# Kernel tuning notes

Hardware: AMD Instinct MI355X
Metric: run time of the kernel (lower is better)

The kernel has to match this reference:

```python
import jax, jax.numpy as jnp
import numpy as np

N = 131072
CODE_DIM = 64
HIDDEN = 128
DT_MAX = 0.125
N_STEPS = 8  # = ceil(max|t1-t2| / DT_MAX); extra steps are exact no-ops since dt=0 for finished rows


def setup_inputs() -> dict:
    key = jax.random.key(0)
    ks = jax.random.split(key, 8)
    deform_code = jax.random.normal(ks[0], (N, CODE_DIM), dtype=jnp.float32)
    pos_init = jax.random.normal(ks[1], (N, 3), dtype=jnp.float32)
    t1 = jax.random.uniform(ks[2], (N, 1), dtype=jnp.float32)
    t2 = jnp.zeros((N, 1), dtype=jnp.float32)
    # vel_net MLP params: concat(code, xyzt)[68] -> 128 -> 128 -> 3, tanh activations
    s1 = 1.0 / np.sqrt(CODE_DIM + 4)
    s2 = 1.0 / np.sqrt(HIDDEN)
    W1 = jax.random.normal(ks[3], (CODE_DIM + 4, HIDDEN), dtype=jnp.float32) * s1
    b1 = jnp.zeros((HIDDEN,), dtype=jnp.float32)
    W2 = jax.random.normal(ks[4], (HIDDEN, HIDDEN), dtype=jnp.float32) * s2
    b2 = jnp.zeros((HIDDEN,), dtype=jnp.float32)
    W3 = jax.random.normal(ks[5], (HIDDEN, 3), dtype=jnp.float32) * s2
    b3 = jnp.zeros((3,), dtype=jnp.float32)
    return {"deform_code": deform_code, "pos_init": pos_init, "t1": t1, "t2": t2,
            "W1": W1, "b1": b1, "W2": W2, "b2": b2, "W3": W3, "b3": b3}


def reference(deform_code, pos_init, t1, t2, W1, b1, W2, b2, W3, b3):
    def get_vel(code, xyzt):  # works for single sample or batch
        x = jnp.concatenate([code, xyzt], axis=-1)
        h = jnp.tanh(x @ W1 + b1)
        h = jnp.tanh(h @ W2 + b2)
        return h @ W3 + b3

    def u_func(code, xyzt):  # per-sample, for jacobian wrt xyzt (argnums=1)
        u = get_vel(code, xyzt)
        return u, u

    jac_fn = jax.vmap(jax.jacrev(u_func, argnums=1, has_aux=True))  # [N,3,4] jac, [N,3] vel

    n = pos_init.shape[0]
    deform0 = jnp.broadcast_to(jnp.eye(3, dtype=pos_init.dtype), (n, 3, 3))

    def step(state, _):
        xyz, t_curr, offset, deform = state
        # dt == 0 exactly for finished rows -> all updates below are no-ops (matches masked in-place updates)
        dt = jnp.sign(offset) * jnp.minimum(jnp.abs(offset), DT_MAX)  # [N,1]
        v0 = get_vel(deform_code, jnp.concatenate([xyz, t_curr], axis=-1))
        p_mid = xyz - 0.5 * dt * v0
        t_mid = t_curr - 0.5 * dt
        jac_v, velocity = jac_fn(deform_code, jnp.concatenate([p_mid, t_mid], axis=-1))
        drotdt = jnp.einsum('noi,nij->noj', jac_v[:, :3, :3], deform)
        deform = deform - dt[..., None] * drotdt
        xyz = xyz - dt * velocity
        return (xyz, t_curr - dt, offset - dt, deform), None

    state0 = (pos_init, t1, t1 - t2, deform0)
    (xyz, _, _, deform), _ = jax.lax.scan(step, state0, None, length=N_STEPS)
    return xyz, deform
```

## Files before the change

### kernel.cpp

```cpp
#include <hip/hip_runtime.h>
#include <hip/hip_bf16.h>

#define H 128
#define NSTEPS 8
#define DT_MAXF 0.125f
#define WAVES 4
#define PPW 16
#define PPB (WAVES*PPW)
#define WPACK_U4 4992

typedef __attribute__((ext_vector_type(8))) short short8;
typedef __attribute__((ext_vector_type(4))) float floatx4;
typedef __attribute__((ext_vector_type(2))) float f32x2;

__device__ __forceinline__ f32x2 sp2(float v) { return (f32x2){v, v}; }
__device__ __forceinline__ f32x2 fma2(f32x2 a, f32x2 b, f32x2 c) {
    return __builtin_elementwise_fma(a, b, c);
}
__device__ __forceinline__ f32x2 tanh2(f32x2 x) {
    f32x2 y = x * 2.8853900817779268f;
    f32x2 e; e[0] = __builtin_amdgcn_exp2f(y[0]); e[1] = __builtin_amdgcn_exp2f(y[1]);
    f32x2 ep = e + 1.0f;
    float rt = __builtin_amdgcn_rcpf(ep[0] * ep[1]);
    f32x2 eps = __builtin_shufflevector(ep, ep, 1, 0);
    f32x2 r = eps * sp2(rt);
    return fma2(sp2(-2.0f), r, sp2(1.0f));
}
__device__ __forceinline__ unsigned f2bf(float x) {
    unsigned u = __float_as_uint(x);
    return (u + 0x7FFFu + ((u >> 16) & 1u)) >> 16;
}
__device__ __forceinline__ unsigned pk2(float a, float b) {
    union { __hip_bfloat162 h; unsigned u; } U;
    U.h = __float22bfloat162_rn(make_float2(a, b));
    return U.u;
}
__device__ __forceinline__ unsigned pkv(f32x2 v) { return pk2(v[0], v[1]); }
__device__ __forceinline__ short8 mk8(unsigned a, unsigned b, unsigned c, unsigned d) {
    union { unsigned u[4]; short8 s; } U;
    U.u[0] = a; U.u[1] = b; U.u[2] = c; U.u[3] = d; return U.s;
}
__device__ __forceinline__ short8 xyzt_frag(float x, float y, float z, float t, int q) {
    unsigned hx = f2bf(x), hy = f2bf(y), hz = f2bf(z), ht = f2bf(t);
    float lx = x - __uint_as_float(hx << 16);
    float ly = y - __uint_as_float(hy << 16);
    float lz = z - __uint_as_float(hz << 16);
    float lt = t - __uint_as_float(ht << 16);
    unsigned w0 = hx | (hy << 16), w1 = hz | (ht << 16);
    unsigned w2 = pk2(lx, ly),     w3 = pk2(lz, lt);
    union { unsigned u[4]; short8 s; } F;
    F.u[0] = (q < 2)  ? w0 : 0u;
    F.u[1] = (q < 2)  ? w1 : 0u;
    F.u[2] = (q == 0) ? w2 : 0u;
    F.u[3] = (q == 0) ? w3 : 0u;
    return F.s;
}

__device__ __forceinline__ int step_bucket(float t1v, float t2v) {
    float off = fabsf(t1v - t2v);
    int b = (int)ceilf(off * 8.0f);
    return min(max(b, 0), 8);
}
__global__ void prep_hist(const float* __restrict__ t1g, const float* __restrict__ t2g,
                          unsigned* cnt, int N) {
    __shared__ unsigned h[9];
    if (threadIdx.x < 9) h[threadIdx.x] = 0u;
    __syncthreads();
    int i = blockIdx.x * 256 + threadIdx.x;
    if (i < N) atomicAdd(&h[step_bucket(t1g[i], t2g[i])], 1u);
    __syncthreads();
    if (threadIdx.x < 9 && h[threadIdx.x]) atomicAdd(&cnt[threadIdx.x], h[threadIdx.x]);
}
__global__ void prep_prefix(unsigned* cnt) {
    if (threadIdx.x == 0) {
        unsigned run = 0;
        for (int b = 8; b >= 0; --b) { unsigned c = cnt[b]; cnt[9 + b] = run; run += c; }
    }
}
__global__ void prep_scatter(const float* __restrict__ t1g, const float* __restrict__ t2g,
                             unsigned* cnt, int* __restrict__ perm, int N) {
    __shared__ unsigned h[9];
    __shared__ unsigned base[9];
    if (threadIdx.x < 9) h[threadIdx.x] = 0u;
    __syncthreads();
    int i = blockIdx.x * 256 + threadIdx.x;
    int b = 0; unsigned r = 0;
    if (i < N) {
        b = step_bucket(t1g[i], t2g[i]);
        r = atomicAdd(&h[b], 1u);
    }
    __syncthreads();
    if (threadIdx.x < 9 && h[threadIdx.x])
        base[threadIdx.x] = atomicAdd(&cnt[9 + threadIdx.x], h[threadIdx.x]);
    __syncthreads();
    if (i < N) perm[base[b] + r] = i;
}

__global__ void prep_pack(const float* __restrict__ W1, const float* __restrict__ W2,
                          const float* __restrict__ W3, const float* __restrict__ b2,
                          uint4* __restrict__ wp) {
    const int gid = blockIdx.x * 256 + threadIdx.x;
    const int stride = gridDim.x * 256;
    for (int e = gid; e < 1024; e += stride) {
        int t = e >> 7, rem = e & 127;
        int c = rem >> 6, l = rem & 63;
        int qq = l >> 4, mm = l & 15;
        int u = t*16 + mm;
        int g0 = c*32 + qq*4, g1 = g0 + 16;
        unsigned hh[8]; float lo[8];
        #pragma unroll
        for (int j = 0; j < 4; ++j) {
            float w0 = W1[(g0+j)*H + u];
            float w1 = W1[(g1+j)*H + u];
            hh[j]   = f2bf(w0); lo[j]   = w0 - __uint_as_float(hh[j]   << 16);
            hh[4+j] = f2bf(w1); lo[4+j] = w1 - __uint_as_float(hh[4+j] << 16);
        }
        wp[((t*2+c)*2+0)*64 + l] = make_uint4(hh[0]|(hh[1]<<16), hh[2]|(hh[3]<<16),
                                              hh[4]|(hh[5]<<16), hh[6]|(hh[7]<<16));
        wp[((t*2+c)*2+1)*64 + l] = make_uint4(pk2(lo[0],lo[1]), pk2(lo[2],lo[3]),
                                              pk2(lo[4],lo[5]), pk2(lo[6],lo[7]));
    }
    for (int ch = gid; ch < 2048; ch += stride) {
        int ln = ch & 63, ts = ch >> 6;
        int s = ts & 3, t = ts >> 2;
        int qq = ln >> 4, n = t*16 + (ln & 15);
        int u0 = s*32 + qq*4, u1 = u0 + 16;
        unsigned w0 = f2bf(W2[(u0+0)*H+n]) | (f2bf(W2[(u0+1)*H+n]) << 16);
        unsigned w1 = f2bf(W2[(u0+2)*H+n]) | (f2bf(W2[(u0+3)*H+n]) << 16);
        unsigned w2 = f2bf(W2[(u1+0)*H+n]) | (f2bf(W2[(u1+1)*H+n]) << 16);
        unsigned w3v = f2bf(W2[(u1+2)*H+n]) | (f2bf(W2[(u1+3)*H+n]) << 16);
        wp[2048 + ch] = make_uint4(w0, w1, w2, w3v);
    }
    for (int e = gid; e < 512; e += stride) {
        int t = e >> 6, l = e & 63;
        int u = t*16 + (l & 15), qq = l >> 4;
        unsigned hb[4], lb[4];
        #pragma unroll
        for (int c = 0; c < 4; ++c) {
            float wv = W1[(64 + c)*H + u];
            unsigned hh = f2bf(wv);
            float wl = wv - __uint_as_float(hh << 16);
            hb[c] = hh; lb[c] = f2bf(wl);
        }
        unsigned hi01 = hb[0] | (hb[1] << 16), hi23 = hb[2] | (hb[3] << 16);
        unsigned lo01 = lb[0] | (lb[1] << 16), lo23 = lb[2] | (lb[3] << 16);
        uint4 o;
        if (qq == 0)      o = make_uint4(hi01, hi23, hi01, hi23);
        else if (qq == 1) o = make_uint4(lo01, lo23, 0u, 0u);
        else              o = make_uint4(0u, 0u, 0u, 0u);
        wp[4096 + e] = o;
    }
    for (int e = gid; e < 256; e += stride) {
        int s = e >> 6, l = e & 63;
        int a = l & 15, qq = l >> 4;
        uint4 o = make_uint4(0u, 0u, 0u, 0u);
        if (a < 3) {
            int u0 = s*32 + qq*4, u1 = u0 + 16;
            o.x = f2bf(W3[(u0+0)*3+a]) | (f2bf(W3[(u0+1)*3+a]) << 16);
            o.y = f2bf(W3[(u0+2)*3+a]) | (f2bf(W3[(u0+3)*3+a]) << 16);
            o.z = f2bf(W3[(u1+0)*3+a]) | (f2bf(W3[(u1+1)*3+a]) << 16);
            o.w = f2bf(W3[(u1+2)*3+a]) | (f2bf(W3[(u1+3)*3+a]) << 16);
        }
        wp[4608 + e] = o;
    }
    for (int i = gid; i < 128; i += stride) {
        int sec = i >> 5, k = i & 31;
        float4 v = (sec < 3) ? ((const float4*)(W1 + (size_t)(64+sec)*H))[k]
                             : ((const float4*)b2)[k];
        wp[4864 + i] = *(const uint4*)&v;
    }
}

__global__ __launch_bounds__(256, 2)
void velwarp(const float* __restrict__ code, const float* __restrict__ pos,
             const float* __restrict__ t1g, const float* __restrict__ t2g,
             const float* __restrict__ W1, const float* __restrict__ b1,
             const float* __restrict__ W2, const float* __restrict__ b2,
             const float* __restrict__ W3, const float* __restrict__ b3,
             float* __restrict__ out, const int* __restrict__ perm,
             const uint4* __restrict__ wpack, int N)
{
    __shared__ __align__(16) uint4 WbufU[2048];
    __shared__ __align__(16) uint4 W1AU[8*64];
    __shared__ __align__(16) uint4 W3AU[4*64];
    __shared__ __align__(16) floatx4 WdX4[32];
    __shared__ __align__(16) floatx4 WdY4[32];
    __shared__ __align__(16) floatx4 WdZ4[32];
    __shared__ __align__(16) floatx4 b2C4[32];

    const int tid = threadIdx.x;
    const int L   = tid & 63;
    const int m   = L & 15;
    const int q   = L >> 4;
    const int pb  = blockIdx.x * PPB + (tid >> 6) * PPW;
    const int p   = perm ? perm[pb + m] : (pb + m);

    if (wpack) {
        #pragma unroll 4
        for (int i = tid; i < 2048; i += 256) WbufU[i] = wpack[i];
        #pragma unroll 2
        for (int i = tid; i < 512; i += 256) W1AU[i] = wpack[4096 + i];
        W3AU[tid < 256 ? tid : 0] = wpack[4608 + (tid < 256 ? tid : 0)];
        if (tid < 128) {
            int sec = tid >> 5, k = tid & 31;
            uint4 v = wpack[4864 + tid];
            floatx4 f = *(const floatx4*)&v;
            if (sec == 0)      WdX4[k] = f;
            else if (sec == 1) WdY4[k] = f;
            else if (sec == 2) WdZ4[k] = f;
            else               b2C4[k] = f;
        }
    } else {
        for (int e = tid; e < 1024; e += 256) {
            int t = e >> 7, rem = e & 127;
            int c = rem >> 6, l = rem & 63;
            int qq = l >> 4, mm = l & 15;
            int u = t*16 + mm;
            int g0 = c*32 + qq*4, g1 = g0 + 16;
            unsigned hh[8]; float lo[8];
            #pragma unroll
            for (int j = 0; j < 4; ++j) {
                float w0 = W1[(g0+j)*H + u];
                float w1 = W1[(g1+j)*H + u];
                hh[j]   = f2bf(w0); lo[j]   = w0 - __uint_as_float(hh[j]   << 16);
                hh[4+j] = f2bf(w1); lo[4+j] = w1 - __uint_as_float(hh[4+j] << 16);
            }
            WbufU[((t*2+c)*2+0)*64 + l] = make_uint4(hh[0]|(hh[1]<<16), hh[2]|(hh[3]<<16),
                                                     hh[4]|(hh[5]<<16), hh[6]|(hh[7]<<16));
            WbufU[((t*2+c)*2+1)*64 + l] = make_uint4(pk2(lo[0],lo[1]), pk2(lo[2],lo[3]),
                                                     pk2(lo[4],lo[5]), pk2(lo[6],lo[7]));
        }
        for (int e = tid; e < 512; e += 256) {
            int t = e >> 6, l = e & 63;
            int u = t*16 + (l & 15), qq = l >> 4;
            unsigned hb[4], lb[4];
            #pragma unroll
            for (int c = 0; c < 4; ++c) {
                float wv = W1[(64 + c)*H + u];
                unsigned hh = f2bf(wv);
                float wl = wv - __uint_as_float(hh << 16);
                hb[c] = hh; lb[c] = f2bf(wl);
            }
            unsigned hi01 = hb[0] | (hb[1] << 16), hi23 = hb[2] | (hb[3] << 16);
            unsigned lo01 = lb[0] | (lb[1] << 16), lo23 = lb[2] | (lb[3] << 16);
            uint4 o;
            if (qq == 0)      o = make_uint4(hi01, hi23, hi01, hi23);
            else if (qq == 1) o = make_uint4(lo01, lo23, 0u, 0u);
            else              o = make_uint4(0u, 0u, 0u, 0u);
            W1AU[e] = o;
        }
        for (int e = tid; e < 256; e += 256) {
            int s = e >> 6, l = e & 63;
            int a = l & 15, qq = l >> 4;
            uint4 o = make_uint4(0u, 0u, 0u, 0u);
            if (a < 3) {
                int u0 = s*32 + qq*4, u1 = u0 + 16;
                o.x = f2bf(W3[(u0+0)*3+a]) | (f2bf(W3[(u0+1)*3+a]) << 16);
                o.y = f2bf(W3[(u0+2)*3+a]) | (f2bf(W3[(u0+3)*3+a]) << 16);
                o.z = f2bf(W3[(u1+0)*3+a]) | (f2bf(W3[(u1+1)*3+a]) << 16);
                o.w = f2bf(W3[(u1+2)*3+a]) | (f2bf(W3[(u1+3)*3+a]) << 16);
            }
            W3AU[e] = o;
        }
        if (tid < 32) {
            WdX4[tid] = ((const floatx4*)(W1 + (size_t)64*H))[tid];
            WdY4[tid] = ((const floatx4*)(W1 + (size_t)65*H))[tid];
            WdZ4[tid] = ((const floatx4*)(W1 + (size_t)66*H))[tid];
            b2C4[tid] = ((const floatx4*)b2)[tid];
        }
    }
    __syncthreads();

    floatx4 base1C[8];
    {
        const float4* crow4 = (const float4*)(code + (size_t)p * 64);
        short8 Bh[2], Bl[2];
        #pragma unroll
        for (int c = 0; c < 2; ++c) {
            float4 a = crow4[c*8 + q];
            float4 b = crow4[c*8 + 4 + q];
            unsigned h0 = f2bf(a.x), h1 = f2bf(a.y), h2 = f2bf(a.z), h3 = f2bf(a.w);
            unsigned g0 = f2bf(b.x), g1 = f2bf(b.y), g2 = f2bf(b.z), g3 = f2bf(b.w);
            float l0 = a.x - __uint_as_float(h0<<16), l1 = a.y - __uint_as_float(h1<<16);
            float l2 = a.z - __uint_as_float(h2<<16), l3 = a.w - __uint_as_float(h3<<16);
            float m0 = b.x - __uint_as_float(g0<<16), m1 = b.y - __uint_as_float(g1<<16);
            float m2 = b.z - __uint_as_float(g2<<16), m3 = b.w - __uint_as_float(g3<<16);
            Bh[c] = mk8(h0|(h1<<16), h2|(h3<<16), g0|(g1<<16), g2|(g3<<16));
            Bl[c] = mk8(pk2(l0,l1), pk2(l2,l3), pk2(m0,m1), pk2(m2,m3));
        }
        const short8* Wb = (const short8*)WbufU;
        #pragma unroll
        for (int t = 0; t < 8; ++t) {
            floatx4 z = *(const floatx4*)&b1[t*16 + q*4];
            short8 Wh0 = Wb[((t*2+0)*2+0)*64 + L];
            short8 Wh1 = Wb[((t*2+1)*2+0)*64 + L];
            short8 Wl0 = Wb[((t*2+0)*2+1)*64 + L];
            short8 Wl1 = Wb[((t*2+1)*2+1)*64 + L];
            z = __builtin_amdgcn_mfma_f32_16x16x32_bf16(Wh0, Bh[0], z, 0, 0, 0);
            z = __builtin_amdgcn_mfma_f32_16x16x32_bf16(Wh1, Bh[1], z, 0, 0, 0);
            z = __builtin_amdgcn_mfma_f32_16x16x32_bf16(Wh0, Bl[0], z, 0, 0, 0);
            z = __builtin_amdgcn_mfma_f32_16x16x32_bf16(Wh1, Bl[1], z, 0, 0, 0);
            z = __builtin_amdgcn_mfma_f32_16x16x32_bf16(Wl0, Bh[0], z, 0, 0, 0);
            z = __builtin_amdgcn_mfma_f32_16x16x32_bf16(Wl1, Bh[1], z, 0, 0, 0);
            base1C[t] = z;
        }
    }
    __syncthreads();

    if (wpack) {
        #pragma unroll 4
        for (int i = tid; i < 2048; i += 256) WbufU[i] = wpack[2048 + i];
    } else {
        for (int ch = tid; ch < 2048; ch += 256) {
            int ln = ch & 63, ts = ch >> 6;
            int s = ts & 3, t = ts >> 2;
            int qq = ln >> 4, n = t*16 + (ln & 15);
            int u0 = s*32 + qq*4, u1 = u0 + 16;
            unsigned w0 = f2bf(W2[(u0+0)*H+n]) | (f2bf(W2[(u0+1)*H+n]) << 16);
            unsigned w1 = f2bf(W2[(u0+2)*H+n]) | (f2bf(W2[(u0+3)*H+n]) << 16);
            unsigned w2 = f2bf(W2[(u1+0)*H+n]) | (f2bf(W2[(u1+1)*H+n]) << 16);
            unsigned w3v = f2bf(W2[(u1+2)*H+n]) | (f2bf(W2[(u1+3)*H+n]) << 16);
            WbufU[ch] = make_uint4(w0, w1, w2, w3v);
        }
    }

    float px_ = pos[p*3+0], py_ = pos[p*3+1], pz_ = pos[p*3+2];
    float tc_ = t1g[p];
    float off_ = tc_ - t2g[p];
    f32x2 Dp[3]; float Ds[3];
    Dp[0] = (f32x2){1.f, 0.f}; Ds[0] = 0.f;
    Dp[1] = (f32x2){0.f, 1.f}; Ds[1] = 0.f;
    Dp[2] = (f32x2){0.f, 0.f}; Ds[2] = 1.f;
    const float b30 = b3[0], b31 = b3[1], b32 = b3[2];
    __syncthreads();

    const short8* Bf   = (const short8*)WbufU;
    const short8* W1Af = (const short8*)W1AU;
    const short8* W3Af = (const short8*)W3AU;
    const floatx4 Z4 = {0.f, 0.f, 0.f, 0.f};

    for (int step = 0; step < NSTEPS; ++step) {
        if (!__any(off_ != 0.0f)) break;

        float vAx, vAy, vAz;
        {
            short8 xf = xyzt_frag(px_, py_, pz_, tc_, q);
            floatx4 z[8];
            #pragma unroll
            for (int t = 0; t < 8; ++t)
                z[t] = __builtin_amdgcn_mfma_f32_16x16x32_bf16(W1Af[t*64 + L], xf, base1C[t], 0, 0, 0);
            short8 fh[4];
            #pragma unroll
            for (int s = 0; s < 4; ++s) {
                f32x2 a0 = tanh2(z[2*s].xy),   a1 = tanh2(z[2*s].zw);
                f32x2 c0 = tanh2(z[2*s+1].xy), c1 = tanh2(z[2*s+1].zw);
                fh[s] = mk8(pkv(a0), pkv(a1), pkv(c0), pkv(c1));
            }
            __builtin_amdgcn_sched_barrier(0);
            floatx4 vacc = Z4;
            #pragma unroll
            for (int qi = 0; qi < 4; ++qi) {
                const int T0 = 2*qi, T1 = 2*qi + 1;
                floatx4 acc0 = __builtin_amdgcn_mfma_f32_16x16x32_bf16(
                    Bf[(T0*4 + 0)*64 + L], fh[0], b2C4[T0*4 + q], 0, 0, 0);
                floatx4 acc1 = __builtin_amdgcn_mfma_f32_16x16x32_bf16(
                    Bf[(T1*4 + 0)*64 + L], fh[0], b2C4[T1*4 + q], 0, 0, 0);
                #pragma unroll
                for (int s = 1; s < 4; ++s) {
                    acc0 = __builtin_amdgcn_mfma_f32_16x16x32_bf16(Bf[(T0*4 + s)*64 + L], fh[s], acc0, 0, 0, 0);
                    acc1 = __builtin_amdgcn_mfma_f32_16x16x32_bf16(Bf[(T1*4 + s)*64 + L], fh[s], acc1, 0, 0, 0);
                }
                f32x2 e00 = tanh2(acc0.xy), e01 = tanh2(acc0.zw);
                f32x2 e10 = tanh2(acc1.xy), e11 = tanh2(acc1.zw);
                short8 ef = mk8(pkv(e00), pkv(e01), pkv(e10), pkv(e11));
                vacc = __builtin_amdgcn_mfma_f32_16x16x32_bf16(W3Af[qi*64 + L], ef, vacc, 0, 0, 0);
                __builtin_amdgcn_sched_barrier(0);
            }
            vAx = __shfl(vacc[0], m, 64);
            vAy = __shfl(vacc[1], m, 64);
            vAz = __shfl(vacc[2], m, 64);
        }

        float dt_ = copysignf(fminf(fabsf(off_), DT_MAXF), off_);
        float hd = 0.5f * dt_;
        float mx = px_ - hd*(vAx + b30);
        float my = py_ - hd*(vAy + b31);
        float mz = pz_ - hd*(vAz + b32);
        float tm = tc_ - hd;

        float vx, vy, vz;
        floatx4 V = Z4, J0 = Z4, J1 = Z4, J2 = Z4;
        {
            short8 xf = xyzt_frag(mx, my, mz, tm, q);
            floatx4 z[8];
            #pragma unroll
            for (int t = 0; t < 8; ++t)
                z[t] = __builtin_amdgcn_mfma_f32_16x16x32_bf16(W1Af[t*64 + L], xf, base1C[t], 0, 0, 0);
            short8 fh[4], fd0[4], fd1[4], fd2[4];
            #pragma unroll
            for (int s = 0; s < 4; ++s) {
                unsigned uh[4], u0[4], u1[4], u2[4];
                #pragma unroll
                for (int hf = 0; hf < 2; ++hf) {
                    int t = 2*s + hf;
                    f32x2 h0 = tanh2(z[t].xy), h1 = tanh2(z[t].zw);
                    f32x2 s0 = fma2(-h0, h0, sp2(1.0f));
                    f32x2 s1 = fma2(-h1, h1, sp2(1.0f));
                    floatx4 wx = WdX4[t*4 + q], wy = WdY4[t*4 + q], wz = WdZ4[t*4 + q];
                    uh[2*hf+0] = pkv(h0);         uh[2*hf+1] = pkv(h1);
                    u0[2*hf+0] = pkv(s0 * wx.xy); u0[2*hf+1] = pkv(s1 * wx.zw);
                    u1[2*hf+0] = pkv(s0 * wy.xy); u1[2*hf+1] = pkv(s1 * wy.zw);
                    u2[2*hf+0] = pkv(s0 * wz.xy); u2[2*hf+1] = pkv(s1 * wz.zw);
                }
                fh[s]  = mk8(uh[0], uh[1], uh[2], uh[3]);
                fd0[s] = mk8(u0[0], u0[1], u0[2], u0[3]);
                fd1[s] = mk8(u1[0], u1[1], u1[2], u1[3]);
                fd2[s] = mk8(u2[0], u2[1], u2[2], u2[3]);
            }
            __builtin_amdgcn_sched_barrier(0);
            #pragma unroll
            for (int qi = 0; qi < 4; ++qi) {
                const int T0 = 2*qi, T1 = 2*qi + 1;
                floatx4 aH0, aH1, aD00, aD01, aD10, aD11, aD20, aD21;
                {
                    short8 A0 = Bf[(T0*4 + 0)*64 + L];
                    short8 A1 = Bf[(T1*4 + 0)*64 + L];
                    aH0  = __builtin_amdgcn_mfma_f32_16x16x32_bf16(A0, fh[0],  b2C4[T0*4 + q], 0, 0, 0);
                    aH1  = __builtin_amdgcn_mfma_f32_16x16x32_bf16(A1, fh[0],  b2C4[T1*4 + q], 0, 0, 0);
                    aD00 = __builtin_amdgcn_mfma_f32_16x16x32_bf16(A0, fd0[0], Z4, 0, 0, 0);
                    aD01 = __builtin_amdgcn_mfma_f32_16x16x32_bf16(A1, fd0[0], Z4, 0, 0, 0);
                    aD10 = __builtin_amdgcn_mfma_f32_16x16x32_bf16(A0, fd1[0], Z4, 0, 0, 0);
                    aD11 = __builtin_amdgcn_mfma_f32_16x16x32_bf16(A1, fd1[0], Z4, 0, 0, 0);
                    aD20 = __builtin_amdgcn_mfma_f32_16x16x32_bf16(A0, fd2[0], Z4, 0, 0, 0);
                    aD21 = __builtin_amdgcn_mfma_f32_16x16x32_bf16(A1, fd2[0], Z4, 0, 0, 0);
                }
                #pragma unroll
                for (int s = 1; s < 4; ++s) {
                    short8 A0 = Bf[(T0*4 + s)*64 + L];
                    short8 A1 = Bf[(T1*4 + s)*64 + L];
                    aH0  = __builtin_amdgcn_mfma_f32_16x16x32_bf16(A0, fh[s],  aH0,  0, 0, 0);
                    aH1  = __builtin_amdgcn_mfma_f32_16x16x32_bf16(A1, fh[s],  aH1,  0, 0, 0);
                    aD00 = __builtin_amdgcn_mfma_f32_16x16x32_bf16(A0, fd0[s], aD00, 0, 0, 0);
                    aD01 = __builtin_amdgcn_mfma_f32_16x16x32_bf16(A1, fd0[s], aD01, 0, 0, 0);
                    aD10 = __builtin_amdgcn_mfma_f32_16x16x32_bf16(A0, fd1[s], aD10, 0, 0, 0);
                    aD11 = __builtin_amdgcn_mfma_f32_16x16x32_bf16(A1, fd1[s], aD11, 0, 0, 0);
                    aD20 = __builtin_amdgcn_mfma_f32_16x16x32_bf16(A0, fd2[s], aD20, 0, 0, 0);
                    aD21 = __builtin_amdgcn_mfma_f32_16x16x32_bf16(A1, fd2[s], aD21, 0, 0, 0);
                }
                f32x2 h0 = tanh2(aH0.xy), h1 = tanh2(aH0.zw);
                f32x2 h2v = tanh2(aH1.xy), h3 = tanh2(aH1.zw);
                f32x2 s0 = fma2(-h0, h0, sp2(1.0f));
                f32x2 s1 = fma2(-h1, h1, sp2(1.0f));
                f32x2 s2v = fma2(-h2v, h2v, sp2(1.0f));
                f32x2 s3 = fma2(-h3, h3, sp2(1.0f));
                short8 eh = mk8(pkv(h0), pkv(h1), pkv(h2v), pkv(h3));
                short8 e0 = mk8(pkv(s0*aD00.xy), pkv(s1*aD00.zw), pkv(s2v*aD01.xy), pkv(s3*aD01.zw));
                short8 e1 = mk8(pkv(s0*aD10.xy), pkv(s1*aD10.zw), pkv(s2v*aD11.xy), pkv(s3*aD11.zw));
                short8 e2 = mk8(pkv(s0*aD20.xy), pkv(s1*aD20.zw), pkv(s2v*aD21.xy), pkv(s3*aD21.zw));
                const short8 WA = W3Af[qi*64 + L];
                V  = __builtin_amdgcn_mfma_f32_16x16x32_bf16(WA, eh, V,  0, 0, 0);
                J0 = __builtin_amdgcn_mfma_f32_16x16x32_bf16(WA, e0, J0, 0, 0, 0);
                J1 = __builtin_amdgcn_mfma_f32_16x16x32_bf16(WA, e1, J1, 0, 0, 0);
                J2 = __builtin_amdgcn_mfma_f32_16x16x32_bf16(WA, e2, J2, 0, 0, 0);
                __builtin_amdgcn_sched_barrier(0);
            }
            vx = __shfl(V[0], m, 64) + b30;
            vy = __shfl(V[1], m, 64) + b31;
            vz = __shfl(V[2], m, 64) + b32;
        }

        {
            f32x2 ndp[3]; float nds[3];
            #pragma unroll
            for (int o = 0; o < 3; ++o) {
                f32x2 tp = J0[o] * Dp[0];
                tp = fma2(sp2(J1[o]), Dp[1], tp);
                tp = fma2(sp2(J2[o]), Dp[2], tp);
                ndp[o] = fma2(sp2(-dt_), tp, Dp[o]);
                float ts = J0[o]*Ds[0];
                ts = fmaf(J1[o], Ds[1], ts);
                ts = fmaf(J2[o], Ds[2], ts);
                nds[o] = fmaf(-dt_, ts, Ds[o]);
            }
            #pragma unroll
            for (int o = 0; o < 3; ++o) { Dp[o] = ndp[o]; Ds[o] = nds[o]; }
        }
        px_ = fmaf(-dt_, vx, px_);
        py_ = fmaf(-dt_, vy, py_);
        pz_ = fmaf(-dt_, vz, pz_);
        tc_  -= dt_;
        off_ -= dt_;
    }

    if (q == 0) {
        out[p*3+0] = px_; out[p*3+1] = py_; out[p*3+2] = pz_;
        float* o9 = out + (size_t)N*3 + (size_t)p*9;
        #pragma unroll
        for (int o = 0; o < 3; ++o) {
            o9[o*3+0] = Dp[o][0];
            o9[o*3+1] = Dp[o][1];
            o9[o*3+2] = Ds[o];
        }
    }
}

extern "C" void kernel_launch(void* const* d_in, const int* in_sizes, int n_in,
                              void* d_out, int out_size, void* d_ws, size_t ws_size,
                              hipStream_t stream) {
    const float* code = (const float*)d_in[0];
    const float* pos  = (const float*)d_in[1];
    const float* t1   = (const float*)d_in[2];
    const float* t2   = (const float*)d_in[3];
    const float* W1   = (const float*)d_in[4];
    const float* b1   = (const float*)d_in[5];
    const float* W2   = (const float*)d_in[6];
    const float* b2   = (const float*)d_in[7];
    const float* W3   = (const float*)d_in[8];
    const float* b3   = (const float*)d_in[9];
    float* out = (float*)d_out;
    const int N = in_sizes[1] / 3;
    const int blocks = N / PPB;
    const int pblocks = (N + 255) / 256;

    const size_t need_perm = 128 + (size_t)N * sizeof(int);
    const size_t need_full = 128 + (size_t)WPACK_U4 * 16 + (size_t)N * sizeof(int);
    int* perm = nullptr;
    uint4* wpack = nullptr;
    if (d_ws && ws_size >= need_full) {
        unsigned* cnt = (unsigned*)d_ws;
        wpack = (uint4*)((char*)d_ws + 128);
        perm  = (int*)((char*)d_ws + 128 + (size_t)WPACK_U4 * 16);
        hipMemsetAsync(d_ws, 0, 128, stream);
        prep_pack<<<20, 256, 0, stream>>>(W1, W2, W3, b2, wpack);
        prep_hist<<<pblocks, 256, 0, stream>>>(t1, t2, cnt, N);
        prep_prefix<<<1, 64, 0, stream>>>(cnt);
        prep_scatter<<<pblocks, 256, 0, stream>>>(t1, t2, cnt, perm, N);
    } else if (d_ws && ws_size >= need_perm) {
        unsigned* cnt = (unsigned*)d_ws;
        perm = (int*)((char*)d_ws + 128);
        hipMemsetAsync(d_ws, 0, 128, stream);
        prep_hist<<<pblocks, 256, 0, stream>>>(t1, t2, cnt, N);
        prep_prefix<<<1, 64, 0, stream>>>(cnt);
        prep_scatter<<<pblocks, 256, 0, stream>>>(t1, t2, cnt, perm, N);
    }
    velwarp<<<blocks, 256, 0, stream>>>(code, pos, t1, t2, W1, b1, W2, b2, W3, b3,
                                        out, perm, wpack, N);
}
```

Baseline: 272.8 us.

## Fuse prep kernels into two launches and compute layer-1 base from global weights

Replaces the memset plus four prep launches (pack, hist, prefix, scatter) with two kernels. The first kernel computes per-block bucket histograms and does the weight packing in extra blocks. The second kernel has each block rebuild its own exclusive prefix from all block counts, so no global atomics or separate prefix kernel are needed. In the main kernel, the layer-1 code projection now reads packed W1 straight from global memory, which lets W2 be loaded into shared memory once with fewer barriers. The trade-offs are a redundant per-block prefix scan over 512 blocks and uncached global reads of W1 fragments.

```diff
diff --git a/kernel.cpp b/kernel.cpp
--- a/kernel.cpp
+++ b/kernel.cpp
@@ -8,6 +8,8 @@
 #define PPW 16
 #define PPB (WAVES*PPW)
 #define WPACK_U4 4992
+#define HBLK 512
+#define PACKB 20
 
 typedef __attribute__((ext_vector_type(8))) short short8;
 typedef __attribute__((ext_vector_type(4))) float floatx4;
@@ -61,46 +63,11 @@
     int b = (int)ceilf(off * 8.0f);
     return min(max(b, 0), 8);
 }
-__global__ void prep_hist(const float* __restrict__ t1g, const float* __restrict__ t2g,
-                          unsigned* cnt, int N) {
-    __shared__ unsigned h[9];
-    if (threadIdx.x < 9) h[threadIdx.x] = 0u;
-    __syncthreads();
-    int i = blockIdx.x * 256 + threadIdx.x;
-    if (i < N) atomicAdd(&h[step_bucket(t1g[i], t2g[i])], 1u);
-    __syncthreads();
-    if (threadIdx.x < 9 && h[threadIdx.x]) atomicAdd(&cnt[threadIdx.x], h[threadIdx.x]);
-}
-__global__ void prep_prefix(unsigned* cnt) {
-    if (threadIdx.x == 0) {
-        unsigned run = 0;
-        for (int b = 8; b >= 0; --b) { unsigned c = cnt[b]; cnt[9 + b] = run; run += c; }
-    }
-}
-__global__ void prep_scatter(const float* __restrict__ t1g, const float* __restrict__ t2g,
-                             unsigned* cnt, int* __restrict__ perm, int N) {
-    __shared__ unsigned h[9];
-    __shared__ unsigned base[9];
-    if (threadIdx.x < 9) h[threadIdx.x] = 0u;
-    __syncthreads();
-    int i = blockIdx.x * 256 + threadIdx.x;
-    int b = 0; unsigned r = 0;
-    if (i < N) {
-        b = step_bucket(t1g[i], t2g[i]);
-        r = atomicAdd(&h[b], 1u);
-    }
-    __syncthreads();
-    if (threadIdx.x < 9 && h[threadIdx.x])
-        base[threadIdx.x] = atomicAdd(&cnt[9 + threadIdx.x], h[threadIdx.x]);
-    __syncthreads();
-    if (i < N) perm[base[b] + r] = i;
-}
-
-__global__ void prep_pack(const float* __restrict__ W1, const float* __restrict__ W2,
+
+__device__ void pack_body(int gid, int stride,
+                          const float* __restrict__ W1, const float* __restrict__ W2,
                           const float* __restrict__ W3, const float* __restrict__ b2,
                           uint4* __restrict__ wp) {
-    const int gid = blockIdx.x * 256 + threadIdx.x;
-    const int stride = gridDim.x * 256;
     for (int e = gid; e < 1024; e += stride) {
         int t = e >> 7, rem = e & 127;
         int c = rem >> 6, l = rem & 63;
@@ -169,6 +136,91 @@
                              : ((const float4*)b2)[k];
         wp[4864 + i] = *(const uint4*)&v;
     }
+}
+
+__global__ void prep_hist2(const float* __restrict__ t1g, const float* __restrict__ t2g,
+                           unsigned* __restrict__ cnt2, int N, int pblocks,
+                           const float* __restrict__ W1, const float* __restrict__ W2,
+                           const float* __restrict__ W3, const float* __restrict__ b2,
+                           uint4* __restrict__ wp) {
+    if ((int)blockIdx.x >= pblocks) {
+        pack_body((blockIdx.x - pblocks)*256 + threadIdx.x, PACKB*256, W1, W2, W3, b2, wp);
+        return;
+    }
+    __shared__ unsigned h[9];
+    if (threadIdx.x < 9) h[threadIdx.x] = 0u;
+    __syncthreads();
+    int i = blockIdx.x * 256 + threadIdx.x;
+    if (i < N) atomicAdd(&h[step_bucket(t1g[i], t2g[i])], 1u);
+    __syncthreads();
+    if (threadIdx.x < 9) cnt2[blockIdx.x*9 + threadIdx.x] = h[threadIdx.x];
+}
+__global__ void prep_scatter2(const float* __restrict__ t1g, const float* __restrict__ t2g,
+                              const unsigned* __restrict__ cnt2, int* __restrict__ perm,
+                              int N, int pblocks) {
+    __shared__ unsigned cs[HBLK*9];
+    __shared__ unsigned T9[9], O9[9], base9[9], alloc9[9];
+    const int b = blockIdx.x, tid = threadIdx.x;
+    for (int i = tid; i < pblocks*9; i += 256) cs[i] = cnt2[i];
+    if (tid < 9) alloc9[tid] = 0u;
+    __syncthreads();
+    if (tid < 9) {
+        unsigned O = 0, T = 0;
+        for (int i = 0; i < pblocks; ++i) {
+            unsigned c = cs[i*9 + tid];
+            if (i < b) O += c;
+            T += c;
+        }
+        T9[tid] = T; O9[tid] = O;
+    }
+    __syncthreads();
+    if (tid < 9) {
+        unsigned G = 0;
+        for (int k = 8; k > tid; --k) G += T9[k];
+        base9[tid] = G + O9[tid];
+    }
+    __syncthreads();
+    int i = b*256 + tid;
+    if (i < N) {
+        int k = step_bucket(t1g[i], t2g[i]);
+        unsigned r = atomicAdd(&alloc9[k], 1u);
+        perm[base9[k] + r] = i;
+    }
+}
+
+__global__ void prep_hist(const float* __restrict__ t1g, const float* __restrict__ t2g,
+                          unsigned* cnt, int N) {
+    __shared__ unsigned h[9];
+    if (threadIdx.x < 9) h[threadIdx.x] = 0u;
+    __syncthreads();
+    int i = blockIdx.x * 256 + threadIdx.x;
+    if (i < N) atomicAdd(&h[step_bucket(t1g[i], t2g[i])], 1u);
+    __syncthreads();
+    if (threadIdx.x < 9 && h[threadIdx.x]) atomicAdd(&cnt[threadIdx.x], h[threadIdx.x]);
+}
+__global__ void prep_prefix(unsigned* cnt) {
+    if (threadIdx.x == 0) {
+        unsigned run = 0;
+        for (int b = 8; b >= 0; --b) { unsigned c = cnt[b]; cnt[9 + b] = run; run += c; }
+    }
+}
+__global__ void prep_scatter(const float* __restrict__ t1g, const float* __restrict__ t2g,
+                             unsigned* cnt, int* __restrict__ perm, int N) {
+    __shared__ unsigned h[9];
+    __shared__ unsigned base[9];
+    if (threadIdx.x < 9) h[threadIdx.x] = 0u;
+    __syncthreads();
+    int i = blockIdx.x * 256 + threadIdx.x;
+    int b = 0; unsigned r = 0;
+    if (i < N) {
+        b = step_bucket(t1g[i], t2g[i]);
+        r = atomicAdd(&h[b], 1u);
+    }
+    __syncthreads();
+    if (threadIdx.x < 9 && h[threadIdx.x])
+        base[threadIdx.x] = atomicAdd(&cnt[9 + threadIdx.x], h[threadIdx.x]);
+    __syncthreads();
+    if (i < N) perm[base[b] + r] = i;
 }
 
 __global__ __launch_bounds__(256, 2)
@@ -195,12 +247,14 @@
     const int pb  = blockIdx.x * PPB + (tid >> 6) * PPW;
     const int p   = perm ? perm[pb + m] : (pb + m);
 
+    floatx4 base1C[8];
+
     if (wpack) {
         #pragma unroll 4
-        for (int i = tid; i < 2048; i += 256) WbufU[i] = wpack[i];
+        for (int i = tid; i < 2048; i += 256) WbufU[i] = wpack[2048 + i];
         #pragma unroll 2
         for (int i = tid; i < 512; i += 256) W1AU[i] = wpack[4096 + i];
-        W3AU[tid < 256 ? tid : 0] = wpack[4608 + (tid < 256 ? tid : 0)];
+        W3AU[tid & 255] = wpack[4608 + (tid & 255)];
         if (tid < 128) {
             int sec = tid >> 5, k = tid & 31;
             uint4 v = wpack[4864 + tid];
@@ -210,6 +264,40 @@
             else if (sec == 2) WdZ4[k] = f;
             else               b2C4[k] = f;
         }
+        {
+            const float4* crow4 = (const float4*)(code + (size_t)p * 64);
+            short8 Bh[2], Bl[2];
+            #pragma unroll
+            for (int c = 0; c < 2; ++c) {
+                float4 a = crow4[c*8 + q];
+                float4 b = crow4[c*8 + 4 + q];
+                unsigned h0 = f2bf(a.x), h1 = f2bf(a.y), h2 = f2bf(a.z), h3 = f2bf(a.w);
+                unsigned g0 = f2bf(b.x), g1 = f2bf(b.y), g2 = f2bf(b.z), g3 = f2bf(b.w);
+                float l0 = a.x - __uint_as_float(h0<<16), l1 = a.y - __uint_as_float(h1<<16);
+                float l2 = a.z - __uint_as_float(h2<<16), l3 = a.w - __uint_as_float(h3<<16);
+                float m0 = b.x - __uint_as_float(g0<<16), m1 = b.y - __uint_as_float(g1<<16);
+                float m2 = b.z - __uint_as_float(g2<<16), m3 = b.w - __uint_as_float(g3<<16);
+                Bh[c] = mk8(h0|(h1<<16), h2|(h3<<16), g0|(g1<<16), g2|(g3<<16));
+                Bl[c] = mk8(pk2(l0,l1), pk2(l2,l3), pk2(m0,m1), pk2(m2,m3));
+            }
+            const short8* Wb = (const short8*)wpack;
+            #pragma unroll
+            for (int t = 0; t < 8; ++t) {
+                floatx4 z = *(const floatx4*)&b1[t*16 + q*4];
+                short8 Wh0 = Wb[((t*2+0)*2+0)*64 + L];
+                short8 Wh1 = Wb[((t*2+1)*2+0)*64 + L];
+                short8 Wl0 = Wb[((t*2+0)*2+1)*64 + L];
+                short8 Wl1 = Wb[((t*2+1)*2+1)*64 + L];
+                z = __builtin_amdgcn_mfma_f32_16x16x32_bf16(Wh0, Bh[0], z, 0, 0, 0);
+                z = __builtin_amdgcn_mfma_f32_16x16x32_bf16(Wh1, Bh[1], z, 0, 0, 0);
+                z = __builtin_amdgcn_mfma_f32_16x16x32_bf16(Wh0, Bl[0], z, 0, 0, 0);
+                z = __builtin_amdgcn_mfma_f32_16x16x32_bf16(Wh1, Bl[1], z, 0, 0, 0);
+                z = __builtin_amdgcn_mfma_f32_16x16x32_bf16(Wl0, Bh[0], z, 0, 0, 0);
+                z = __builtin_amdgcn_mfma_f32_16x16x32_bf16(Wl1, Bh[1], z, 0, 0, 0);
+                base1C[t] = z;
+            }
+        }
+        __syncthreads();
     } else {
         for (int e = tid; e < 1024; e += 256) {
             int t = e >> 7, rem = e & 127;
@@ -268,49 +356,41 @@
             WdZ4[tid] = ((const floatx4*)(W1 + (size_t)66*H))[tid];
             b2C4[tid] = ((const floatx4*)b2)[tid];
         }
-    }
-    __syncthreads();
-
-    floatx4 base1C[8];
-    {
-        const float4* crow4 = (const float4*)(code + (size_t)p * 64);
-        short8 Bh[2], Bl[2];
-        #pragma unroll
-        for (int c = 0; c < 2; ++c) {
-            float4 a = crow4[c*8 + q];
-            float4 b = crow4[c*8 + 4 + q];
-            unsigned h0 = f2bf(a.x), h1 = f2bf(a.y), h2 = f2bf(a.z), h3 = f2bf(a.w);
-            unsigned g0 = f2bf(b.x), g1 = f2bf(b.y), g2 = f2bf(b.z), g3 = f2bf(b.w);
-            float l0 = a.x - __uint_as_float(h0<<16), l1 = a.y - __uint_as_float(h1<<16);
-            float l2 = a.z - __uint_as_float(h2<<16), l3 = a.w - __uint_as_float(h3<<16);
-            float m0 = b.x - __uint_as_float(g0<<16), m1 = b.y - __uint_as_float(g1<<16);
-            float m2 = b.z - __uint_as_float(g2<<16), m3 = b.w - __uint_as_float(g3<<16);
-            Bh[c] = mk8(h0|(h1<<16), h2|(h3<<16), g0|(g1<<16), g2|(g3<<16));
-            Bl[c] = mk8(pk2(l0,l1), pk2(l2,l3), pk2(m0,m1), pk2(m2,m3));
-        }
-        const short8* Wb = (const short8*)WbufU;
-        #pragma unroll
-        for (int t = 0; t < 8; ++t) {
-            floatx4 z = *(const floatx4*)&b1[t*16 + q*4];
-            short8 Wh0 = Wb[((t*2+0)*2+0)*64 + L];
-            short8 Wh1 = Wb[((t*2+1)*2+0)*64 + L];
-            short8 Wl0 = Wb[((t*2+0)*2+1)*64 + L];
-            short8 Wl1 = Wb[((t*2+1)*2+1)*64 + L];
-            z = __builtin_amdgcn_mfma_f32_16x16x32_bf16(Wh0, Bh[0], z, 0, 0, 0);
-            z = __builtin_amdgcn_mfma_f32_16x16x32_bf16(Wh1, Bh[1], z, 0, 0, 0);
-            z = __builtin_amdgcn_mfma_f32_16x16x32_bf16(Wh0, Bl[0], z, 0, 0, 0);
-            z = __builtin_amdgcn_mfma_f32_16x16x32_bf16(Wh1, Bl[1], z, 0, 0, 0);
-            z = __builtin_amdgcn_mfma_f32_16x16x32_bf16(Wl0, Bh[0], z, 0, 0, 0);
-            z = __builtin_amdgcn_mfma_f32_16x16x32_bf16(Wl1, Bh[1], z, 0, 0, 0);
-            base1C[t] = z;
-        }
-    }
-    __syncthreads();
-
-    if (wpack) {
-        #pragma unroll 4
-        for (int i = tid; i < 2048; i += 256) WbufU[i] = wpack[2048 + i];
-    } else {
+        __syncthreads();
+        {
+            const float4* crow4 = (const float4*)(code + (size_t)p * 64);
+            short8 Bh[2], Bl[2];
+            #pragma unroll
+            for (int c = 0; c < 2; ++c) {
+                float4 a = crow4[c*8 + q];
+                float4 b = crow4[c*8 + 4 + q];
+                unsigned h0 = f2bf(a.x), h1 = f2bf(a.y), h2 = f2bf(a.z), h3 = f2bf(a.w);
+                unsigned g0 = f2bf(b.x), g1 = f2bf(b.y), g2 = f2bf(b.z), g3 = f2bf(b.w);
+                float l0 = a.x - __uint_as_float(h0<<16), l1 = a.y - __uint_as_float(h1<<16);
+                float l2 = a.z - __uint_as_float(h2<<16), l3 = a.w - __uint_as_float(h3<<16);
+                float m0 = b.x - __uint_as_float(g0<<16), m1 = b.y - __uint_as_float(g1<<16);
+                float m2 = b.z - __uint_as_float(g2<<16), m3 = b.w - __uint_as_float(g3<<16);
+                Bh[c] = mk8(h0|(h1<<16), h2|(h3<<16), g0|(g1<<16), g2|(g3<<16));
+                Bl[c] = mk8(pk2(l0,l1), pk2(l2,l3), pk2(m0,m1), pk2(m2,m3));
+            }
+            const short8* Wb = (const short8*)WbufU;
+            #pragma unroll
+            for (int t = 0; t < 8; ++t) {
+                floatx4 z = *(const floatx4*)&b1[t*16 + q*4];
+                short8 Wh0 = Wb[((t*2+0)*2+0)*64 + L];
+                short8 Wh1 = Wb[((t*2+1)*2+0)*64 + L];
+                short8 Wl0 = Wb[((t*2+0)*2+1)*64 + L];
+                short8 Wl1 = Wb[((t*2+1)*2+1)*64 + L];
+                z = __builtin_amdgcn_mfma_f32_16x16x32_bf16(Wh0, Bh[0], z, 0, 0, 0);
+                z = __builtin_amdgcn_mfma_f32_16x16x32_bf16(Wh1, Bh[1], z, 0, 0, 0);
+                z = __builtin_amdgcn_mfma_f32_16x16x32_bf16(Wh0, Bl[0], z, 0, 0, 0);
+                z = __builtin_amdgcn_mfma_f32_16x16x32_bf16(Wh1, Bl[1], z, 0, 0, 0);
+                z = __builtin_amdgcn_mfma_f32_16x16x32_bf16(Wl0, Bh[0], z, 0, 0, 0);
+                z = __builtin_amdgcn_mfma_f32_16x16x32_bf16(Wl1, Bh[1], z, 0, 0, 0);
+                base1C[t] = z;
+            }
+        }
+        __syncthreads();
         for (int ch = tid; ch < 2048; ch += 256) {
             int ln = ch & 63, ts = ch >> 6;
             int s = ts & 3, t = ts >> 2;
@@ -322,6 +402,7 @@
             unsigned w3v = f2bf(W2[(u1+2)*H+n]) | (f2bf(W2[(u1+3)*H+n]) << 16);
             WbufU[ch] = make_uint4(w0, w1, w2, w3v);
         }
+        __syncthreads();
     }
 
     float px_ = pos[p*3+0], py_ = pos[p*3+1], pz_ = pos[p*3+2];
@@ -332,7 +413,6 @@
     Dp[1] = (f32x2){0.f, 1.f}; Ds[1] = 0.f;
     Dp[2] = (f32x2){0.f, 0.f}; Ds[2] = 1.f;
     const float b30 = b3[0], b31 = b3[1], b32 = b3[2];
-    __syncthreads();
 
     const short8* Bf   = (const short8*)WbufU;
     const short8* W1Af = (const short8*)W1AU;
@@ -522,19 +602,18 @@
     const int blocks = N / PPB;
     const int pblocks = (N + 255) / 256;
 
-    const size_t need_perm = 128 + (size_t)N * sizeof(int);
-    const size_t need_full = 128 + (size_t)WPACK_U4 * 16 + (size_t)N * sizeof(int);
+    const size_t pb9 = ((size_t)pblocks * 9 * 4 + 15) & ~(size_t)15;
+    const size_t need_full = pb9 + (size_t)WPACK_U4 * 16 + (size_t)N * 4;
+    const size_t need_perm = 128 + (size_t)N * 4;
     int* perm = nullptr;
     uint4* wpack = nullptr;
-    if (d_ws && ws_size >= need_full) {
-        unsigned* cnt = (unsigned*)d_ws;
-        wpack = (uint4*)((char*)d_ws + 128);
-        perm  = (int*)((char*)d_ws + 128 + (size_t)WPACK_U4 * 16);
-        hipMemsetAsync(d_ws, 0, 128, stream);
-        prep_pack<<<20, 256, 0, stream>>>(W1, W2, W3, b2, wpack);
-        prep_hist<<<pblocks, 256, 0, stream>>>(t1, t2, cnt, N);
-        prep_prefix<<<1, 64, 0, stream>>>(cnt);
-        prep_scatter<<<pblocks, 256, 0, stream>>>(t1, t2, cnt, perm, N);
+    if (d_ws && ws_size >= need_full && pblocks <= HBLK) {
+        unsigned* cnt2 = (unsigned*)d_ws;
+        wpack = (uint4*)((char*)d_ws + pb9);
+        perm  = (int*)((char*)d_ws + pb9 + (size_t)WPACK_U4 * 16);
+        prep_hist2<<<pblocks + PACKB, 256, 0, stream>>>(t1, t2, cnt2, N, pblocks,
+                                                        W1, W2, W3, b2, wpack);
+        prep_scatter2<<<pblocks, 256, 0, stream>>>(t1, t2, cnt2, perm, N, pblocks);
     } else if (d_ws && ws_size >= need_perm) {
         unsigned* cnt = (unsigned*)d_ws;
         perm = (int*)((char*)d_ws + 128);
```

Result: faster. 263.4 us (-3.5%).
